# Kernel tuning notes

Measured on AMD Instinct MI355X. Metric: run time of the kernel, lower is better.

## Reference

```python
import jax, jax.numpy as jnp
import numpy as np

NODE_DIM = 128
N_NODES = 100000
N_EDGES = 600000


def setup_inputs() -> dict:
    key = jax.random.key(0)
    k_x, k_e, k_w1, k_b1, k_w2, k_b2 = jax.random.split(key, 6)
    x = jax.random.normal(k_x, (N_NODES, NODE_DIM), dtype=jnp.float32)
    edge_index = jax.random.randint(k_e, (2, N_EDGES), 0, N_NODES, dtype=jnp.int64)
    # nn.Linear default init: U(-1/sqrt(fan_in), 1/sqrt(fan_in))
    lim1 = 1.0 / np.sqrt(2 * NODE_DIM)
    W1 = jax.random.uniform(k_w1, (2 * NODE_DIM, NODE_DIM), minval=-lim1, maxval=lim1, dtype=jnp.float32)
    b1 = jax.random.uniform(k_b1, (NODE_DIM,), minval=-lim1, maxval=lim1, dtype=jnp.float32)
    lim2 = 1.0 / np.sqrt(NODE_DIM)
    W2 = jax.random.uniform(k_w2, (NODE_DIM, 1), minval=-lim2, maxval=lim2, dtype=jnp.float32)
    b2 = jax.random.uniform(k_b2, (1,), minval=-lim2, maxval=lim2, dtype=jnp.float32)
    return {"x": x, "edge_index": edge_index, "W1": W1, "b1": b1, "W2": W2, "b2": b2}


def reference(x, edge_index, W1, b1, W2, b2):
    src = edge_index[0]
    dst = edge_index[1]
    # [E, 2*node_dim] gathered pair features
    pair = jnp.concatenate([x[src], x[dst]], axis=-1)
    h = jax.nn.relu(pair @ W1 + b1)          # [E, node_dim]
    s = jax.nn.sigmoid(h @ W2 + b2)          # [E, 1]
    return s.squeeze(-1)                      # [E]
```

## Files before the change

### kernel.cpp

```cpp
#include <hip/hip_runtime.h>
#include <hip/hip_bf16.h>
#include <stdint.h>

#define NODE_DIM 128
#define N_NODES  100000
#define N_EDGES  600000
#define NOUT     256

#define QSTEP_INV 64.0f
#define QSTEP     (1.0f / 64.0f)

typedef __bf16 bf16x8 __attribute__((ext_vector_type(8)));
typedef float  f32x4  __attribute__((ext_vector_type(4)));

static __device__ inline unsigned pack2_bf16(float a, float b) {
    unsigned short ua = __builtin_bit_cast(unsigned short, (__bf16)a);
    unsigned short ub = __builtin_bit_cast(unsigned short, (__bf16)b);
    return (unsigned)ua | ((unsigned)ub << 16);
}

static __device__ __forceinline__ void async_copy16(const float* g, void* l) {
    __builtin_amdgcn_global_load_lds(
        (__attribute__((address_space(1))) void*)(uintptr_t)g,
        (__attribute__((address_space(3))) void*)(uint32_t)(uintptr_t)l,
        16, 0, 0);
}

__global__ void wprep_kernel(const float* __restrict__ W1, __bf16* __restrict__ Wt) {
    int i = blockIdx.x * 256 + threadIdx.x;
    if (i >= NOUT * NODE_DIM) return;
    int kp = i >> 7;
    int n  = i & 127;
    float v = W1[i];
    int np = (kp < NODE_DIM) ? n  : (n + NODE_DIM);
    int k  = (kp < NODE_DIM) ? kp : (kp - NODE_DIM);
    Wt[np * NODE_DIM + k] = (__bf16)v;
}

#define MT   64
#define ELD  264

__global__ __launch_bounds__(256)
void gemm_pre_kernel(const float* __restrict__ x, const __bf16* __restrict__ Wt,
                     const float* __restrict__ b1,
                     unsigned char* __restrict__ Ai, unsigned char* __restrict__ Bi) {
    __shared__ __align__(16) char lds_raw[MT * ELD * 2];
    const float* Xf = (const float*)lds_raw;
    __bf16 (*Ls)[ELD] = (__bf16 (*)[ELD])lds_raw;

    const int t    = threadIdx.x;
    const int wave = t >> 6;
    const int lane = t & 63;
    const int lm   = lane & 15;
    const int q    = lane >> 4;
    const int m0   = blockIdx.x * MT;
    const int n0   = wave * 64;

#pragma unroll
    for (int i = 0; i < 8; ++i) {
        const int sbase = i * 256 + wave * 64;
        const int s  = sbase + lane;
        const int R  = s >> 5;
        const int p  = s & 31;
        const int cg = p ^ (R & 7);
        int gr = m0 + R;
        if (gr > N_NODES - 1) gr = N_NODES - 1;
        async_copy16(x + (size_t)gr * NODE_DIM + cg * 4, lds_raw + (size_t)sbase * 16);
    }

    bf16x8 bfr[4][4];
#pragma unroll
    for (int nt = 0; nt < 4; ++nt) {
        const int n = n0 + nt * 16 + lm;
#pragma unroll
        for (int ks = 0; ks < 4; ++ks)
            bfr[nt][ks] = __builtin_bit_cast(bf16x8,
                *(const uint4*)(Wt + (size_t)n * NODE_DIM + ks * 32 + q * 8));
    }

    __syncthreads();

    f32x4 acc[4][4];
#pragma unroll
    for (int a = 0; a < 4; ++a)
#pragma unroll
        for (int b = 0; b < 4; ++b)
            acc[a][b] = (f32x4){0.f, 0.f, 0.f, 0.f};

#pragma unroll
    for (int mt = 0; mt < 4; ++mt) {
        const int R  = mt * 16 + lm;
        const int rs = R & 7;
#pragma unroll
        for (int ks = 0; ks < 4; ++ks) {
            const int c0 = ks * 8 + q * 2;
            const float4 f0 = *(const float4*)&Xf[(R * 32 + (c0 ^ rs)) * 4];
            const float4 f1 = *(const float4*)&Xf[(R * 32 + ((c0 + 1) ^ rs)) * 4];
            uint4 p;
            p.x = pack2_bf16(f0.x, f0.y);
            p.y = pack2_bf16(f0.z, f0.w);
            p.z = pack2_bf16(f1.x, f1.y);
            p.w = pack2_bf16(f1.z, f1.w);
            bf16x8 af = __builtin_bit_cast(bf16x8, p);
#pragma unroll
            for (int nt = 0; nt < 4; ++nt)
                acc[mt][nt] = __builtin_amdgcn_mfma_f32_16x16x32_bf16(
                    af, bfr[nt][ks], acc[mt][nt], 0, 0, 0);
        }
    }

    __syncthreads();

#pragma unroll
    for (int nt = 0; nt < 4; ++nt) {
        const int n = n0 + nt * 16 + lm;
        const float bias = (n < NODE_DIM) ? b1[n] : 0.f;
#pragma unroll
        for (int mt = 0; mt < 4; ++mt) {
#pragma unroll
            for (int r = 0; r < 4; ++r)
                Ls[mt * 16 + q * 4 + r][n] = (__bf16)(acc[mt][nt][r] + bias);
        }
    }
    __syncthreads();

    const int grp = t >> 4;
    const int sub = t & 15;
#pragma unroll
    for (int pass = 0; pass < 8; ++pass) {
        const int hr   = pass * 16 + grp;
        const int row  = hr >> 1;
        const int half = hr & 1;
        const uint4 v = *(const uint4*)(&Ls[row][half * 128 + sub * 8]);
        const unsigned* vu = (const unsigned*)&v;
        unsigned u[8];
#pragma unroll
        for (int i = 0; i < 4; ++i) {
            const float fa = __builtin_bit_cast(float, vu[i] << 16);
            const float fb = __builtin_bit_cast(float, vu[i] & 0xffff0000u);
            float ga = fmaf(fa, QSTEP_INV, 128.5f);
            float gb = fmaf(fb, QSTEP_INV, 128.5f);
            ga = fminf(fmaxf(ga, 0.f), 255.f);
            gb = fminf(fmaxf(gb, 0.f), 255.f);
            u[2 * i]     = (unsigned)ga;
            u[2 * i + 1] = (unsigned)gb;
        }
        uint2 pk;
        pk.x = u[0] | (u[1] << 8) | (u[2] << 16) | (u[3] << 24);
        pk.y = u[4] | (u[5] << 8) | (u[6] << 16) | (u[7] << 24);
        const int m = m0 + row;
        if (m < N_NODES)
            *(uint2*)((half ? Bi : Ai) + (size_t)m * NODE_DIM + sub * 8) = pk;
    }
}

__global__ __launch_bounds__(256)
void edge_score_kernel(const unsigned char* __restrict__ Ai,
                       const unsigned char* __restrict__ Bi,
                       const int* __restrict__ idx,
                       const float* __restrict__ W2, const float* __restrict__ b2,
                       float* __restrict__ out) {
    const int t   = threadIdx.x;
    const int sub = t & 7;
    const int g   = (blockIdx.x * 256 + t) >> 3;
    const int e0  = g * 4;
    if (e0 >= N_EDGES) return;

    float w[16];
#pragma unroll
    for (int j = 0; j < 16; ++j) w[j] = W2[sub * 16 + j];
    const float bias2 = b2[0];

    const int4 sv = *(const int4*)(idx + e0);
    const int4 dv = *(const int4*)(idx + N_EDGES + e0);
    const int s[4] = {sv.x, sv.y, sv.z, sv.w};
    const int d[4] = {dv.x, dv.y, dv.z, dv.w};

    uint4 av[4], bv[4];
#pragma unroll
    for (int i = 0; i < 4; ++i) {
        av[i] = *(const uint4*)(Ai + (size_t)s[i] * NODE_DIM + sub * 16);
        bv[i] = *(const uint4*)(Bi + (size_t)d[i] * NODE_DIM + sub * 16);
    }

    float p[4];
#pragma unroll
    for (int i = 0; i < 4; ++i) {
        const unsigned aw[4] = {av[i].x, av[i].y, av[i].z, av[i].w};
        const unsigned bw[4] = {bv[i].x, bv[i].y, bv[i].z, bv[i].w};
        float acc = 0.f;
#pragma unroll
        for (int wd = 0; wd < 4; ++wd) {
#pragma unroll
            for (int k = 0; k < 4; ++k) {
                const int ua = (int)((aw[wd] >> (8 * k)) & 0xffu);
                const int ub = (int)((bw[wd] >> (8 * k)) & 0xffu);
                const int r  = max(ua + ub, 256) - 256;
                acc = fmaf((float)r, w[wd * 4 + k], acc);
            }
        }
        p[i] = acc;
    }

#pragma unroll
    for (int i = 0; i < 4; ++i) {
        p[i] += __shfl_xor(p[i], 1);
        p[i] += __shfl_xor(p[i], 2);
        p[i] += __shfl_xor(p[i], 4);
    }

    if (sub == 0) {
        float4 o;
        o.x = 1.f / (1.f + __expf(-fmaf(p[0], QSTEP, bias2)));
        o.y = 1.f / (1.f + __expf(-fmaf(p[1], QSTEP, bias2)));
        o.z = 1.f / (1.f + __expf(-fmaf(p[2], QSTEP, bias2)));
        o.w = 1.f / (1.f + __expf(-fmaf(p[3], QSTEP, bias2)));
        *(float4*)(out + e0) = o;
    }
}

__global__ __launch_bounds__(128)
void naive_edge_kernel(const float* __restrict__ x, const int* __restrict__ idx,
                       const float* __restrict__ W1, const float* __restrict__ b1,
                       const float* __restrict__ W2, const float* __restrict__ b2,
                       float* __restrict__ out) {
    __shared__ float pair[2 * NODE_DIM];
    __shared__ float red[2];
    int e = blockIdx.x;
    int t = threadIdx.x;
    int s = idx[e], d = idx[N_EDGES + e];
    pair[t]            = x[(size_t)s * NODE_DIM + t];
    pair[NODE_DIM + t] = x[(size_t)d * NODE_DIM + t];
    __syncthreads();
    float acc = b1[t];
    for (int k = 0; k < 2 * NODE_DIM; ++k)
        acc = fmaf(pair[k], W1[k * NODE_DIM + t], acc);
    float c = fmaxf(acc, 0.f) * W2[t];
#pragma unroll
    for (int m = 1; m < 64; m <<= 1) c += __shfl_xor(c, m);
    if ((t & 63) == 0) red[t >> 6] = c;
    __syncthreads();
    if (t == 0) out[e] = 1.f / (1.f + __expf(-(red[0] + red[1] + b2[0])));
}

extern "C" void kernel_launch(void* const* d_in, const int* in_sizes, int n_in,
                              void* d_out, int out_size, void* d_ws, size_t ws_size,
                              hipStream_t stream) {
    const float* x   = (const float*)d_in[0];
    const int*   idx = (const int*)d_in[1];
    const float* W1  = (const float*)d_in[2];
    const float* b1  = (const float*)d_in[3];
    const float* W2  = (const float*)d_in[4];
    const float* b2  = (const float*)d_in[5];
    float* out = (float*)d_out;

    const size_t tab_bytes = (size_t)N_NODES * NODE_DIM;
    const size_t wt_bytes  = (size_t)NOUT * NODE_DIM * sizeof(__bf16);
    const size_t need = 2 * tab_bytes + wt_bytes;

    if (ws_size >= need) {
        unsigned char* Ai = (unsigned char*)d_ws;
        unsigned char* Bi = Ai + tab_bytes;
        __bf16* Wt = (__bf16*)(Bi + tab_bytes);
        hipLaunchKernelGGL(wprep_kernel, dim3(128), dim3(256), 0, stream, W1, Wt);
        hipLaunchKernelGGL(gemm_pre_kernel, dim3((N_NODES + MT - 1) / MT), dim3(256),
                           0, stream, x, Wt, b1, Ai, Bi);
        hipLaunchKernelGGL(edge_score_kernel, dim3((N_EDGES / 4 + 31) / 32), dim3(256),
                           0, stream, Ai, Bi, idx, W2, b2, out);
    } else {
        hipLaunchKernelGGL(naive_edge_kernel, dim3(N_EDGES), dim3(128), 0, stream,
                           x, idx, W1, b1, W2, b2, out);
    }
}
```

Before: 132.9 us.

## Bucket-sort edges by source node to improve gather locality

Adds histogram, scan and scatter kernels that bucket edges by source node (64 nodes per bucket) into permuted src/dst/original-index arrays. The edge scoring kernel then reads edges in bucketed order so source-row gathers hit cache, and it remaps its block order across 8 groups, presumably to spread work across XCDs. Outputs are scattered back through the original index. This costs three extra launches, atomics and extra index traffic, and the output stores become scattered 4-byte writes instead of float4 stores.

```diff
diff --git a/kernel.cpp b/kernel.cpp
--- a/kernel.cpp
+++ b/kernel.cpp
@@ -9,6 +9,9 @@
 
 #define QSTEP_INV 64.0f
 #define QSTEP     (1.0f / 64.0f)
+
+#define BSHIFT 6
+#define NBUK   1563
 
 typedef __bf16 bf16x8 __attribute__((ext_vector_type(8)));
 typedef float  f32x4  __attribute__((ext_vector_type(4)));
@@ -26,8 +29,10 @@
         16, 0, 0);
 }
 
-__global__ void wprep_kernel(const float* __restrict__ W1, __bf16* __restrict__ Wt) {
+__global__ void wprep_kernel(const float* __restrict__ W1, __bf16* __restrict__ Wt,
+                             int* __restrict__ hzero) {
     int i = blockIdx.x * 256 + threadIdx.x;
+    if (i < 2 * NBUK) hzero[i] = 0;
     if (i >= NOUT * NODE_DIM) return;
     int kp = i >> 7;
     int n  = i & 127;
@@ -155,14 +160,77 @@
 }
 
 __global__ __launch_bounds__(256)
+void ehist_kernel(const int* __restrict__ idx, int* __restrict__ hist) {
+    __shared__ int h[NBUK];
+    for (int i = threadIdx.x; i < NBUK; i += 256) h[i] = 0;
+    __syncthreads();
+    const int stride = gridDim.x * 256;
+    for (int e = blockIdx.x * 256 + threadIdx.x; e < N_EDGES; e += stride)
+        atomicAdd(&h[idx[e] >> BSHIFT], 1);
+    __syncthreads();
+    for (int i = threadIdx.x; i < NBUK; i += 256) {
+        const int c = h[i];
+        if (c) atomicAdd(&hist[i], c);
+    }
+}
+
+#define SEG 7
+__global__ __launch_bounds__(256)
+void escan_kernel(const int* __restrict__ hist, int* __restrict__ cursor) {
+    __shared__ int partial[256];
+    const int t = threadIdx.x;
+    int v[SEG];
+    int s = 0;
+#pragma unroll
+    for (int j = 0; j < SEG; ++j) {
+        const int i = t * SEG + j;
+        v[j] = (i < NBUK) ? hist[i] : 0;
+        s += v[j];
+    }
+    partial[t] = s;
+    __syncthreads();
+    for (int off = 1; off < 256; off <<= 1) {
+        const int add = (t >= off) ? partial[t - off] : 0;
+        __syncthreads();
+        partial[t] += add;
+        __syncthreads();
+    }
+    int run = partial[t] - s;
+#pragma unroll
+    for (int j = 0; j < SEG; ++j) {
+        const int i = t * SEG + j;
+        if (i < NBUK) cursor[i] = run;
+        run += v[j];
+    }
+}
+
+__global__ __launch_bounds__(256)
+void escatter_kernel(const int* __restrict__ idx, int* __restrict__ cursor,
+                     int* __restrict__ se, int* __restrict__ de,
+                     int* __restrict__ oe) {
+    const int stride = gridDim.x * 256;
+    for (int e = blockIdx.x * 256 + threadIdx.x; e < N_EDGES; e += stride) {
+        const int s = idx[e];
+        const int p = atomicAdd(&cursor[s >> BSHIFT], 1);
+        se[p] = s;
+        de[p] = idx[N_EDGES + e];
+        oe[p] = e;
+    }
+}
+
+__global__ __launch_bounds__(256)
 void edge_score_kernel(const unsigned char* __restrict__ Ai,
                        const unsigned char* __restrict__ Bi,
-                       const int* __restrict__ idx,
+                       const int* __restrict__ se, const int* __restrict__ de,
+                       const int* __restrict__ oe,
                        const float* __restrict__ W2, const float* __restrict__ b2,
                        float* __restrict__ out) {
+    const int q8  = (int)gridDim.x >> 3;
+    const int bid = (blockIdx.x & 7) * q8 + (blockIdx.x >> 3);
+
     const int t   = threadIdx.x;
     const int sub = t & 7;
-    const int g   = (blockIdx.x * 256 + t) >> 3;
+    const int g   = (bid * 256 + t) >> 3;
     const int e0  = g * 4;
     if (e0 >= N_EDGES) return;
 
@@ -171,8 +239,8 @@
     for (int j = 0; j < 16; ++j) w[j] = W2[sub * 16 + j];
     const float bias2 = b2[0];
 
-    const int4 sv = *(const int4*)(idx + e0);
-    const int4 dv = *(const int4*)(idx + N_EDGES + e0);
+    const int4 sv = *(const int4*)(se + e0);
+    const int4 dv = *(const int4*)(de + e0);
     const int s[4] = {sv.x, sv.y, sv.z, sv.w};
     const int d[4] = {dv.x, dv.y, dv.z, dv.w};
 
@@ -210,12 +278,11 @@
     }
 
     if (sub == 0) {
-        float4 o;
-        o.x = 1.f / (1.f + __expf(-fmaf(p[0], QSTEP, bias2)));
-        o.y = 1.f / (1.f + __expf(-fmaf(p[1], QSTEP, bias2)));
-        o.z = 1.f / (1.f + __expf(-fmaf(p[2], QSTEP, bias2)));
-        o.w = 1.f / (1.f + __expf(-fmaf(p[3], QSTEP, bias2)));
-        *(float4*)(out + e0) = o;
+        const int4 ov = *(const int4*)(oe + e0);
+        out[ov.x] = 1.f / (1.f + __expf(-fmaf(p[0], QSTEP, bias2)));
+        out[ov.y] = 1.f / (1.f + __expf(-fmaf(p[1], QSTEP, bias2)));
+        out[ov.z] = 1.f / (1.f + __expf(-fmaf(p[2], QSTEP, bias2)));
+        out[ov.w] = 1.f / (1.f + __expf(-fmaf(p[3], QSTEP, bias2)));
     }
 }
 
@@ -254,19 +321,31 @@
     const float* b2  = (const float*)d_in[5];
     float* out = (float*)d_out;
 
-    const size_t tab_bytes = (size_t)N_NODES * NODE_DIM;
-    const size_t wt_bytes  = (size_t)NOUT * NODE_DIM * sizeof(__bf16);
-    const size_t need = 2 * tab_bytes + wt_bytes;
+    const size_t tab_bytes  = (size_t)N_NODES * NODE_DIM;
+    const size_t wt_bytes   = (size_t)NOUT * NODE_DIM * sizeof(__bf16);
+    const size_t edge_bytes = (size_t)N_EDGES * sizeof(int);
+    const size_t buk_bytes  = (size_t)NBUK * sizeof(int);
+    const size_t need = 2 * tab_bytes + wt_bytes + 3 * edge_bytes + 2 * buk_bytes;
 
     if (ws_size >= need) {
         unsigned char* Ai = (unsigned char*)d_ws;
         unsigned char* Bi = Ai + tab_bytes;
-        __bf16* Wt = (__bf16*)(Bi + tab_bytes);
-        hipLaunchKernelGGL(wprep_kernel, dim3(128), dim3(256), 0, stream, W1, Wt);
+        __bf16* Wt  = (__bf16*)(Bi + tab_bytes);
+        int* se     = (int*)((char*)Wt + wt_bytes);
+        int* de     = se + N_EDGES;
+        int* oe     = de + N_EDGES;
+        int* hist   = oe + N_EDGES;
+        int* cursor = hist + NBUK;
+
+        hipLaunchKernelGGL(wprep_kernel, dim3(128), dim3(256), 0, stream, W1, Wt, hist);
         hipLaunchKernelGGL(gemm_pre_kernel, dim3((N_NODES + MT - 1) / MT), dim3(256),
                            0, stream, x, Wt, b1, Ai, Bi);
+        hipLaunchKernelGGL(ehist_kernel, dim3(256), dim3(256), 0, stream, idx, hist);
+        hipLaunchKernelGGL(escan_kernel, dim3(1), dim3(256), 0, stream, hist, cursor);
+        hipLaunchKernelGGL(escatter_kernel, dim3(256), dim3(256), 0, stream,
+                           idx, cursor, se, de, oe);
         hipLaunchKernelGGL(edge_score_kernel, dim3((N_EDGES / 4 + 31) / 32), dim3(256),
-                           0, stream, Ai, Bi, idx, W2, b2, out);
+                           0, stream, Ai, Bi, se, de, oe, W2, b2, out);
     } else {
         hipLaunchKernelGGL(naive_edge_kernel, dim3(N_EDGES), dim3(128), 0, stream,
                            x, idx, W1, b1, W2, b2, out);
```

After: 240.2 us. +80.8%, slower.

## Pre-convert x to bf16 and make node GEMM persistent with double-buffered LDS

Applied to the files above, without the earlier changes.

Adds a prep kernel that converts x to bf16 alongside the W1 transpose. The node GEMM becomes a persistent kernel with 512 blocks looping over tiles, prefetching the next tile's bf16 rows into a second LDS buffer while computing the current one. This is meant to hide global-load latency and drop the in-loop fp32-to-bf16 conversion. The cost is an extra full pass that writes and rereads x as bf16 in global memory, plus lower occupancy from the larger LDS footprint.

```diff
diff --git a/kernel.cpp b/kernel.cpp
--- a/kernel.cpp
+++ b/kernel.cpp
@@ -19,54 +19,57 @@
     return (unsigned)ua | ((unsigned)ub << 16);
 }
 
-static __device__ __forceinline__ void async_copy16(const float* g, void* l) {
+static __device__ __forceinline__ void async_copy16(const void* g, void* l) {
     __builtin_amdgcn_global_load_lds(
         (__attribute__((address_space(1))) void*)(uintptr_t)g,
         (__attribute__((address_space(3))) void*)(uint32_t)(uintptr_t)l,
         16, 0, 0);
 }
 
-__global__ void wprep_kernel(const float* __restrict__ W1, __bf16* __restrict__ Wt) {
-    int i = blockIdx.x * 256 + threadIdx.x;
-    if (i >= NOUT * NODE_DIM) return;
-    int kp = i >> 7;
-    int n  = i & 127;
-    float v = W1[i];
-    int np = (kp < NODE_DIM) ? n  : (n + NODE_DIM);
-    int k  = (kp < NODE_DIM) ? kp : (kp - NODE_DIM);
-    Wt[np * NODE_DIM + k] = (__bf16)v;
-}
-
-#define MT   64
-#define ELD  264
-
 __global__ __launch_bounds__(256)
-void gemm_pre_kernel(const float* __restrict__ x, const __bf16* __restrict__ Wt,
+void prep_kernel(const float* __restrict__ x, __bf16* __restrict__ xb,
+                 const float* __restrict__ W1, __bf16* __restrict__ Wt) {
+    const int j = blockIdx.x * 256 + threadIdx.x;
+
+    if (j < NOUT * NODE_DIM) {
+        const int kp = j >> 7;
+        const int n  = j & 127;
+        const float v = W1[j];
+        const int np = (kp < NODE_DIM) ? n  : (n + NODE_DIM);
+        const int k  = (kp < NODE_DIM) ? kp : (kp - NODE_DIM);
+        Wt[np * NODE_DIM + k] = (__bf16)v;
+    }
+
+    if (j < N_NODES * NODE_DIM / 8) {
+        const float4 f0 = *(const float4*)(x + (size_t)j * 8);
+        const float4 f1 = *(const float4*)(x + (size_t)j * 8 + 4);
+        uint4 p;
+        p.x = pack2_bf16(f0.x, f0.y);
+        p.y = pack2_bf16(f0.z, f0.w);
+        p.z = pack2_bf16(f1.x, f1.y);
+        p.w = pack2_bf16(f1.z, f1.w);
+        *(uint4*)(xb + (size_t)j * 8) = p;
+    }
+}
+
+#define MT     64
+#define ELD    264
+#define GB     512
+#define NTILES 1563
+
+__global__ __launch_bounds__(256)
+void gemm_pre_kernel(const __bf16* __restrict__ xb, const __bf16* __restrict__ Wt,
                      const float* __restrict__ b1,
                      unsigned char* __restrict__ Ai, unsigned char* __restrict__ Bi) {
-    __shared__ __align__(16) char lds_raw[MT * ELD * 2];
-    const float* Xf = (const float*)lds_raw;
-    __bf16 (*Ls)[ELD] = (__bf16 (*)[ELD])lds_raw;
+    __shared__ __align__(16) char lds_raw[2 * 16384 + MT * ELD * 2];
+    __bf16 (*Ls)[ELD] = (__bf16 (*)[ELD])(lds_raw + 32768);
 
     const int t    = threadIdx.x;
     const int wave = t >> 6;
     const int lane = t & 63;
     const int lm   = lane & 15;
     const int q    = lane >> 4;
-    const int m0   = blockIdx.x * MT;
     const int n0   = wave * 64;
-
-#pragma unroll
-    for (int i = 0; i < 8; ++i) {
-        const int sbase = i * 256 + wave * 64;
-        const int s  = sbase + lane;
-        const int R  = s >> 5;
-        const int p  = s & 31;
-        const int cg = p ^ (R & 7);
-        int gr = m0 + R;
-        if (gr > N_NODES - 1) gr = N_NODES - 1;
-        async_copy16(x + (size_t)gr * NODE_DIM + cg * 4, lds_raw + (size_t)sbase * 16);
-    }
 
     bf16x8 bfr[4][4];
 #pragma unroll
@@ -77,80 +80,117 @@
             bfr[nt][ks] = __builtin_bit_cast(bf16x8,
                 *(const uint4*)(Wt + (size_t)n * NODE_DIM + ks * 32 + q * 8));
     }
-
-    __syncthreads();
-
-    f32x4 acc[4][4];
-#pragma unroll
-    for (int a = 0; a < 4; ++a)
-#pragma unroll
-        for (int b = 0; b < 4; ++b)
-            acc[a][b] = (f32x4){0.f, 0.f, 0.f, 0.f};
-
-#pragma unroll
-    for (int mt = 0; mt < 4; ++mt) {
-        const int R  = mt * 16 + lm;
-        const int rs = R & 7;
-#pragma unroll
-        for (int ks = 0; ks < 4; ++ks) {
-            const int c0 = ks * 8 + q * 2;
-            const float4 f0 = *(const float4*)&Xf[(R * 32 + (c0 ^ rs)) * 4];
-            const float4 f1 = *(const float4*)&Xf[(R * 32 + ((c0 + 1) ^ rs)) * 4];
-            uint4 p;
-            p.x = pack2_bf16(f0.x, f0.y);
-            p.y = pack2_bf16(f0.z, f0.w);
-            p.z = pack2_bf16(f1.x, f1.y);
-            p.w = pack2_bf16(f1.z, f1.w);
-            bf16x8 af = __builtin_bit_cast(bf16x8, p);
-#pragma unroll
-            for (int nt = 0; nt < 4; ++nt)
-                acc[mt][nt] = __builtin_amdgcn_mfma_f32_16x16x32_bf16(
-                    af, bfr[nt][ks], acc[mt][nt], 0, 0, 0);
-        }
-    }
-
-    __syncthreads();
-
+    float bias[4];
 #pragma unroll
     for (int nt = 0; nt < 4; ++nt) {
         const int n = n0 + nt * 16 + lm;
-        const float bias = (n < NODE_DIM) ? b1[n] : 0.f;
+        bias[nt] = (n < NODE_DIM) ? b1[n] : 0.f;
+    }
+
+    auto STAGE = [&](int tile, int ib) {
+        const int m0 = tile * MT;
+#pragma unroll
+        for (int i = 0; i < 4; ++i) {
+            const int s     = i * 256 + wave * 64 + lane;
+            const int sbase = i * 256 + wave * 64;
+            const int R  = s >> 4;
+            const int p  = s & 15;
+            const int cg = p ^ (R & 7);
+            int gr = m0 + R;
+            if (gr > N_NODES - 1) gr = N_NODES - 1;
+            async_copy16((const char*)(xb + (size_t)gr * NODE_DIM) + cg * 16,
+                         lds_raw + (size_t)(ib * 1024 + sbase) * 16);
+        }
+    };
+
+    int tile = blockIdx.x;
+    STAGE(tile, 0);
+    asm volatile("s_waitcnt vmcnt(0)" ::: "memory");
+    __builtin_amdgcn_s_barrier();
+
+    int ib = 0;
+    for (; tile < NTILES; tile += GB, ib ^= 1) {
+        const int m0  = tile * MT;
+        const int nxt = tile + GB;
+
+        asm volatile("s_waitcnt lgkmcnt(0)" ::: "memory");
+        __builtin_amdgcn_s_barrier();
+
+        if (nxt < NTILES) {
+            STAGE(nxt, ib ^ 1);
+            asm volatile("s_waitcnt vmcnt(12)" ::: "memory");
+        } else {
+            asm volatile("s_waitcnt vmcnt(8)" ::: "memory");
+        }
+        __builtin_amdgcn_sched_barrier(0);
+        __builtin_amdgcn_s_barrier();
+
+        f32x4 acc[4][4];
+#pragma unroll
+        for (int a = 0; a < 4; ++a)
+#pragma unroll
+            for (int b = 0; b < 4; ++b)
+                acc[a][b] = (f32x4){0.f, 0.f, 0.f, 0.f};
+
+        const char* xbase = lds_raw + ib * 16384;
 #pragma unroll
         for (int mt = 0; mt < 4; ++mt) {
-#pragma unroll
-            for (int r = 0; r < 4; ++r)
-                Ls[mt * 16 + q * 4 + r][n] = (__bf16)(acc[mt][nt][r] + bias);
-        }
-    }
-    __syncthreads();
-
-    const int grp = t >> 4;
-    const int sub = t & 15;
-#pragma unroll
-    for (int pass = 0; pass < 8; ++pass) {
-        const int hr   = pass * 16 + grp;
-        const int row  = hr >> 1;
-        const int half = hr & 1;
-        const uint4 v = *(const uint4*)(&Ls[row][half * 128 + sub * 8]);
-        const unsigned* vu = (const unsigned*)&v;
-        unsigned u[8];
-#pragma unroll
-        for (int i = 0; i < 4; ++i) {
-            const float fa = __builtin_bit_cast(float, vu[i] << 16);
-            const float fb = __builtin_bit_cast(float, vu[i] & 0xffff0000u);
-            float ga = fmaf(fa, QSTEP_INV, 128.5f);
-            float gb = fmaf(fb, QSTEP_INV, 128.5f);
-            ga = fminf(fmaxf(ga, 0.f), 255.f);
-            gb = fminf(fmaxf(gb, 0.f), 255.f);
-            u[2 * i]     = (unsigned)ga;
-            u[2 * i + 1] = (unsigned)gb;
-        }
-        uint2 pk;
-        pk.x = u[0] | (u[1] << 8) | (u[2] << 16) | (u[3] << 24);
-        pk.y = u[4] | (u[5] << 8) | (u[6] << 16) | (u[7] << 24);
-        const int m = m0 + row;
-        if (m < N_NODES)
+            const int R  = mt * 16 + lm;
+            const int rs = R & 7;
+            const char* rowp = xbase + R * 256;
+#pragma unroll
+            for (int ks = 0; ks < 4; ++ks) {
+                const int c = (ks * 4 + q) ^ rs;
+                const bf16x8 af = __builtin_bit_cast(bf16x8,
+                    *(const uint4*)(rowp + c * 16));
+#pragma unroll
+                for (int nt = 0; nt < 4; ++nt)
+                    acc[mt][nt] = __builtin_amdgcn_mfma_f32_16x16x32_bf16(
+                        af, bfr[nt][ks], acc[mt][nt], 0, 0, 0);
+            }
+        }
+
+#pragma unroll
+        for (int nt = 0; nt < 4; ++nt) {
+            const int n = n0 + nt * 16 + lm;
+#pragma unroll
+            for (int mt = 0; mt < 4; ++mt) {
+#pragma unroll
+                for (int r = 0; r < 4; ++r)
+                    Ls[mt * 16 + q * 4 + r][n] = (__bf16)(acc[mt][nt][r] + bias[nt]);
+            }
+        }
+        asm volatile("s_waitcnt lgkmcnt(0)" ::: "memory");
+        __builtin_amdgcn_s_barrier();
+
+        const int grp = t >> 4;
+        const int sub = t & 15;
+#pragma unroll
+        for (int pass = 0; pass < 8; ++pass) {
+            const int hr   = pass * 16 + grp;
+            const int row  = hr >> 1;
+            const int half = hr & 1;
+            const uint4 v = *(const uint4*)(&Ls[row][half * 128 + sub * 8]);
+            const unsigned* vu = (const unsigned*)&v;
+            unsigned u[8];
+#pragma unroll
+            for (int i = 0; i < 4; ++i) {
+                const float fa = __builtin_bit_cast(float, vu[i] << 16);
+                const float fb = __builtin_bit_cast(float, vu[i] & 0xffff0000u);
+                float ga = fmaf(fa, QSTEP_INV, 128.5f);
+                float gb = fmaf(fb, QSTEP_INV, 128.5f);
+                ga = fminf(fmaxf(ga, 0.f), 255.f);
+                gb = fminf(fmaxf(gb, 0.f), 255.f);
+                u[2 * i]     = (unsigned)ga;
+                u[2 * i + 1] = (unsigned)gb;
+            }
+            uint2 pk;
+            pk.x = u[0] | (u[1] << 8) | (u[2] << 16) | (u[3] << 24);
+            pk.y = u[4] | (u[5] << 8) | (u[6] << 16) | (u[7] << 24);
+            int m = m0 + row;
+            if (m > N_NODES - 1) m = N_NODES - 1;
             *(uint2*)((half ? Bi : Ai) + (size_t)m * NODE_DIM + sub * 8) = pk;
+        }
     }
 }
 
@@ -256,15 +296,19 @@
 
     const size_t tab_bytes = (size_t)N_NODES * NODE_DIM;
     const size_t wt_bytes  = (size_t)NOUT * NODE_DIM * sizeof(__bf16);
-    const size_t need = 2 * tab_bytes + wt_bytes;
+    const size_t xb_bytes  = (size_t)N_NODES * NODE_DIM * sizeof(__bf16);
+    const size_t need = 2 * tab_bytes + wt_bytes + xb_bytes;
 
     if (ws_size >= need) {
         unsigned char* Ai = (unsigned char*)d_ws;
         unsigned char* Bi = Ai + tab_bytes;
         __bf16* Wt = (__bf16*)(Bi + tab_bytes);
-        hipLaunchKernelGGL(wprep_kernel, dim3(128), dim3(256), 0, stream, W1, Wt);
-        hipLaunchKernelGGL(gemm_pre_kernel, dim3((N_NODES + MT - 1) / MT), dim3(256),
-                           0, stream, x, Wt, b1, Ai, Bi);
+        __bf16* xb = (__bf16*)((char*)Wt + wt_bytes);
+
+        hipLaunchKernelGGL(prep_kernel, dim3(N_NODES * NODE_DIM / 8 / 256), dim3(256),
+                           0, stream, x, xb, W1, Wt);
+        hipLaunchKernelGGL(gemm_pre_kernel, dim3(GB), dim3(256),
+                           0, stream, xb, Wt, b1, Ai, Bi);
         hipLaunchKernelGGL(edge_score_kernel, dim3((N_EDGES / 4 + 31) / 32), dim3(256),
                            0, stream, Ai, Bi, idx, W2, b2, out);
     } else {
```

After: 135.0 us. Within noise of the previous version (+1.6%).

## Make node GEMM persistent with double-buffered async LDS prefetch of x tiles

Applied to the files above, without the earlier changes.

Converts the per-node projection kernel from one block per 64-row tile into a persistent grid of 512 blocks that loop over tiles. While one tile is computed, the next tile's x rows are prefetched into a second LDS buffer, with manual vmcnt waits and barriers. W1 fragments and bias are loaded once per block instead of once per tile. The cost is 64KB of LDS per block, which may reduce occupancy, plus fragile hand-written waitcnt synchronisation.

```diff
diff --git a/kernel.cpp b/kernel.cpp
--- a/kernel.cpp
+++ b/kernel.cpp
@@ -19,7 +19,7 @@
     return (unsigned)ua | ((unsigned)ub << 16);
 }
 
-static __device__ __forceinline__ void async_copy16(const float* g, void* l) {
+static __device__ __forceinline__ void async_copy16(const void* g, void* l) {
     __builtin_amdgcn_global_load_lds(
         (__attribute__((address_space(1))) void*)(uintptr_t)g,
         (__attribute__((address_space(3))) void*)(uint32_t)(uintptr_t)l,
@@ -37,36 +37,23 @@
     Wt[np * NODE_DIM + k] = (__bf16)v;
 }
 
-#define MT   64
-#define ELD  264
+#define MT     64
+#define ELD    256
+#define GB     512
+#define NTILES 1563
 
 __global__ __launch_bounds__(256)
 void gemm_pre_kernel(const float* __restrict__ x, const __bf16* __restrict__ Wt,
                      const float* __restrict__ b1,
                      unsigned char* __restrict__ Ai, unsigned char* __restrict__ Bi) {
-    __shared__ __align__(16) char lds_raw[MT * ELD * 2];
-    const float* Xf = (const float*)lds_raw;
-    __bf16 (*Ls)[ELD] = (__bf16 (*)[ELD])lds_raw;
+    __shared__ __align__(16) char lds_raw[2 * 32768];
 
     const int t    = threadIdx.x;
     const int wave = t >> 6;
     const int lane = t & 63;
     const int lm   = lane & 15;
     const int q    = lane >> 4;
-    const int m0   = blockIdx.x * MT;
     const int n0   = wave * 64;
-
-#pragma unroll
-    for (int i = 0; i < 8; ++i) {
-        const int sbase = i * 256 + wave * 64;
-        const int s  = sbase + lane;
-        const int R  = s >> 5;
-        const int p  = s & 31;
-        const int cg = p ^ (R & 7);
-        int gr = m0 + R;
-        if (gr > N_NODES - 1) gr = N_NODES - 1;
-        async_copy16(x + (size_t)gr * NODE_DIM + cg * 4, lds_raw + (size_t)sbase * 16);
-    }
 
     bf16x8 bfr[4][4];
 #pragma unroll
@@ -77,80 +64,126 @@
             bfr[nt][ks] = __builtin_bit_cast(bf16x8,
                 *(const uint4*)(Wt + (size_t)n * NODE_DIM + ks * 32 + q * 8));
     }
-
-    __syncthreads();
-
-    f32x4 acc[4][4];
-#pragma unroll
-    for (int a = 0; a < 4; ++a)
-#pragma unroll
-        for (int b = 0; b < 4; ++b)
-            acc[a][b] = (f32x4){0.f, 0.f, 0.f, 0.f};
-
-#pragma unroll
-    for (int mt = 0; mt < 4; ++mt) {
-        const int R  = mt * 16 + lm;
-        const int rs = R & 7;
-#pragma unroll
-        for (int ks = 0; ks < 4; ++ks) {
-            const int c0 = ks * 8 + q * 2;
-            const float4 f0 = *(const float4*)&Xf[(R * 32 + (c0 ^ rs)) * 4];
-            const float4 f1 = *(const float4*)&Xf[(R * 32 + ((c0 + 1) ^ rs)) * 4];
-            uint4 p;
-            p.x = pack2_bf16(f0.x, f0.y);
-            p.y = pack2_bf16(f0.z, f0.w);
-            p.z = pack2_bf16(f1.x, f1.y);
-            p.w = pack2_bf16(f1.z, f1.w);
-            bf16x8 af = __builtin_bit_cast(bf16x8, p);
-#pragma unroll
-            for (int nt = 0; nt < 4; ++nt)
-                acc[mt][nt] = __builtin_amdgcn_mfma_f32_16x16x32_bf16(
-                    af, bfr[nt][ks], acc[mt][nt], 0, 0, 0);
-        }
-    }
-
-    __syncthreads();
-
+    float bias[4];
 #pragma unroll
     for (int nt = 0; nt < 4; ++nt) {
         const int n = n0 + nt * 16 + lm;
-        const float bias = (n < NODE_DIM) ? b1[n] : 0.f;
+        bias[nt] = (n < NODE_DIM) ? b1[n] : 0.f;
+    }
+
+    auto STAGE = [&](int tile, int ib) {
+        const int m0 = tile * MT;
+#pragma unroll
+        for (int i = 0; i < 8; ++i) {
+            const int s     = i * 256 + wave * 64 + lane;
+            const int sbase = i * 256 + wave * 64;
+            const int R  = s >> 5;
+            const int p  = s & 31;
+            const int cg = p ^ (R & 7);
+            int gr = m0 + R;
+            if (gr > N_NODES - 1) gr = N_NODES - 1;
+            async_copy16(x + (size_t)gr * NODE_DIM + cg * 4,
+                         lds_raw + (size_t)(ib * 2048 + sbase) * 16);
+        }
+    };
+
+    int tile = blockIdx.x;
+    STAGE(tile, 0);
+    asm volatile("s_waitcnt vmcnt(0)" ::: "memory");
+    __builtin_amdgcn_s_barrier();
+
+    int ib = 0;
+    for (; tile < NTILES; tile += GB, ib ^= 1) {
+        const int m0  = tile * MT;
+        const int nxt = tile + GB;
+
+        asm volatile("s_waitcnt lgkmcnt(0)" ::: "memory");
+        __builtin_amdgcn_s_barrier();
+
+        if (nxt < NTILES) {
+            STAGE(nxt, ib ^ 1);
+            asm volatile("s_waitcnt vmcnt(16)" ::: "memory");
+        } else {
+            asm volatile("s_waitcnt vmcnt(8)" ::: "memory");
+        }
+        __builtin_amdgcn_sched_barrier(0);
+        __builtin_amdgcn_s_barrier();
+
+        f32x4 acc[4][4];
+#pragma unroll
+        for (int a = 0; a < 4; ++a)
+#pragma unroll
+            for (int b = 0; b < 4; ++b)
+                acc[a][b] = (f32x4){0.f, 0.f, 0.f, 0.f};
+
+        const float* Xf = (const float*)(lds_raw + ib * 32768);
 #pragma unroll
         for (int mt = 0; mt < 4; ++mt) {
-#pragma unroll
-            for (int r = 0; r < 4; ++r)
-                Ls[mt * 16 + q * 4 + r][n] = (__bf16)(acc[mt][nt][r] + bias);
-        }
-    }
-    __syncthreads();
-
-    const int grp = t >> 4;
-    const int sub = t & 15;
-#pragma unroll
-    for (int pass = 0; pass < 8; ++pass) {
-        const int hr   = pass * 16 + grp;
-        const int row  = hr >> 1;
-        const int half = hr & 1;
-        const uint4 v = *(const uint4*)(&Ls[row][half * 128 + sub * 8]);
-        const unsigned* vu = (const unsigned*)&v;
-        unsigned u[8];
-#pragma unroll
-        for (int i = 0; i < 4; ++i) {
-            const float fa = __builtin_bit_cast(float, vu[i] << 16);
-            const float fb = __builtin_bit_cast(float, vu[i] & 0xffff0000u);
-            float ga = fmaf(fa, QSTEP_INV, 128.5f);
-            float gb = fmaf(fb, QSTEP_INV, 128.5f);
-            ga = fminf(fmaxf(ga, 0.f), 255.f);
-            gb = fminf(fmaxf(gb, 0.f), 255.f);
-            u[2 * i]     = (unsigned)ga;
-            u[2 * i + 1] = (unsigned)gb;
-        }
-        uint2 pk;
-        pk.x = u[0] | (u[1] << 8) | (u[2] << 16) | (u[3] << 24);
-        pk.y = u[4] | (u[5] << 8) | (u[6] << 16) | (u[7] << 24);
-        const int m = m0 + row;
-        if (m < N_NODES)
+            const int R  = mt * 16 + lm;
+            const int rs = R & 7;
+#pragma unroll
+            for (int ks = 0; ks < 4; ++ks) {
+                const int c0 = ks * 8 + q * 2;
+                const float4 f0 = *(const float4*)&Xf[(R * 32 + (c0 ^ rs)) * 4];
+                const float4 f1 = *(const float4*)&Xf[(R * 32 + ((c0 + 1) ^ rs)) * 4];
+                uint4 p;
+                p.x = pack2_bf16(f0.x, f0.y);
+                p.y = pack2_bf16(f0.z, f0.w);
+                p.z = pack2_bf16(f1.x, f1.y);
+                p.w = pack2_bf16(f1.z, f1.w);
+                bf16x8 af = __builtin_bit_cast(bf16x8, p);
+#pragma unroll
+                for (int nt = 0; nt < 4; ++nt)
+                    acc[mt][nt] = __builtin_amdgcn_mfma_f32_16x16x32_bf16(
+                        af, bfr[nt][ks], acc[mt][nt], 0, 0, 0);
+            }
+        }
+
+        asm volatile("s_waitcnt lgkmcnt(0)" ::: "memory");
+        __builtin_amdgcn_s_barrier();
+
+        __bf16 (*Ls)[ELD] = (__bf16 (*)[ELD])(lds_raw + ib * 32768);
+#pragma unroll
+        for (int nt = 0; nt < 4; ++nt) {
+            const int n = n0 + nt * 16 + lm;
+#pragma unroll
+            for (int mt = 0; mt < 4; ++mt) {
+#pragma unroll
+                for (int r = 0; r < 4; ++r)
+                    Ls[mt * 16 + q * 4 + r][n] = (__bf16)(acc[mt][nt][r] + bias[nt]);
+            }
+        }
+        asm volatile("s_waitcnt lgkmcnt(0)" ::: "memory");
+        __builtin_amdgcn_s_barrier();
+
+        const int grp = t >> 4;
+        const int sub = t & 15;
+#pragma unroll
+        for (int pass = 0; pass < 8; ++pass) {
+            const int hr   = pass * 16 + grp;
+            const int row  = hr >> 1;
+            const int half = hr & 1;
+            const uint4 v = *(const uint4*)(&Ls[row][half * 128 + sub * 8]);
+            const unsigned* vu = (const unsigned*)&v;
+            unsigned u[8];
+#pragma unroll
+            for (int i = 0; i < 4; ++i) {
+                const float fa = __builtin_bit_cast(float, vu[i] << 16);
+                const float fb = __builtin_bit_cast(float, vu[i] & 0xffff0000u);
+                float ga = fmaf(fa, QSTEP_INV, 128.5f);
+                float gb = fmaf(fb, QSTEP_INV, 128.5f);
+                ga = fminf(fmaxf(ga, 0.f), 255.f);
+                gb = fminf(fmaxf(gb, 0.f), 255.f);
+                u[2 * i]     = (unsigned)ga;
+                u[2 * i + 1] = (unsigned)gb;
+            }
+            uint2 pk;
+            pk.x = u[0] | (u[1] << 8) | (u[2] << 16) | (u[3] << 24);
+            pk.y = u[4] | (u[5] << 8) | (u[6] << 16) | (u[7] << 24);
+            int m = m0 + row;
+            if (m > N_NODES - 1) m = N_NODES - 1;
             *(uint2*)((half ? Bi : Ai) + (size_t)m * NODE_DIM + sub * 8) = pk;
+        }
     }
 }
 
@@ -263,7 +296,7 @@
         unsigned char* Bi = Ai + tab_bytes;
         __bf16* Wt = (__bf16*)(Bi + tab_bytes);
         hipLaunchKernelGGL(wprep_kernel, dim3(128), dim3(256), 0, stream, W1, Wt);
-        hipLaunchKernelGGL(gemm_pre_kernel, dim3((N_NODES + MT - 1) / MT), dim3(256),
+        hipLaunchKernelGGL(gemm_pre_kernel, dim3(GB), dim3(256),
                            0, stream, x, Wt, b1, Ai, Bi);
         hipLaunchKernelGGL(edge_score_kernel, dim3((N_EDGES / 4 + 31) / 32), dim3(256),
                            0, stream, Ai, Bi, idx, W2, b2, out);
```

Measured after the change: 130.7 us. Within noise of the previous version (-1.6%).
